# Performance work log

Hardware: AMD Instinct MI355X
Metric: run time of the kernel (lower is better)

## Reference

```python
import jax, jax.numpy as jnp
import numpy as np

WS = 7          # window_size
NH = 12         # num_heads
EPS = 1e-5      # LayerNorm eps


def setup_inputs() -> dict:
    key = jax.random.key(0)
    ks = jax.random.split(key, 8)
    B, H, W, C = 32, 56, 56, 384
    x = jax.random.normal(ks[0], (B, H * W, C), dtype=jnp.float32)
    s = 1.0 / np.sqrt(C)
    return {
        "x": x,
        "ln_gamma": jnp.ones((C,), jnp.float32),
        "ln_beta": jnp.zeros((C,), jnp.float32),
        "w_in": jax.random.normal(ks[1], (3 * C, C), jnp.float32) * s,   # torch in_proj_weight
        "b_in": jnp.zeros((3 * C,), jnp.float32),
        "w_out": jax.random.normal(ks[2], (C, C), jnp.float32) * s,      # torch out_proj.weight
        "b_out": jnp.zeros((C,), jnp.float32),
        "H": H,
        "W": W,
    }


def reference(x, ln_gamma, ln_beta, w_in, b_in, w_out, b_out, H, W):
    B, N, C = x.shape
    assert N == H * W
    hd = C // NH
    shortcut = x

    # LayerNorm
    mu = jnp.mean(x, axis=-1, keepdims=True)
    var = jnp.mean((x - mu) ** 2, axis=-1, keepdims=True)
    y = (x - mu) * jax.lax.rsqrt(var + EPS) * ln_gamma + ln_beta

    # window partition (pads are static Python ints)
    y = y.reshape(B, H, W, C)
    pad_h = (WS - H % WS) % WS
    pad_w = (WS - W % WS) % WS
    y = jnp.pad(y, ((0, 0), (0, pad_h), (0, pad_w), (0, 0)))
    Hp, Wp = H + pad_h, W + pad_w
    nh, nw = Hp // WS, Wp // WS
    y = y.reshape(B, nh, WS, nw, WS, C).transpose(0, 1, 3, 2, 4, 5)
    y = y.reshape(B * nh * nw, WS * WS, C)   # [NWIN, L, C]

    # MHA (torch nn.MultiheadAttention, batch_first)
    qkv = y @ w_in.T + b_in                   # [NWIN, L, 3C]
    q, k, v = jnp.split(qkv, 3, axis=-1)
    NWIN, L, _ = y.shape
    q = q.reshape(NWIN, L, NH, hd).transpose(0, 2, 1, 3)
    k = k.reshape(NWIN, L, NH, hd).transpose(0, 2, 1, 3)
    v = v.reshape(NWIN, L, NH, hd).transpose(0, 2, 1, 3)
    scores = jnp.einsum("whqd,whkd->whqk", q, k) / jnp.sqrt(jnp.float32(hd))
    attn = jax.nn.softmax(scores, axis=-1)
    o = jnp.einsum("whqk,whkd->whqd", attn, v)
    o = o.transpose(0, 2, 1, 3).reshape(NWIN, L, C)
    o = o @ w_out.T + b_out

    # window reverse + unpad + residual
    o = o.reshape(B, nh, nw, WS, WS, C).transpose(0, 1, 3, 2, 4, 5)
    o = o.reshape(B, Hp, Wp, C)[:, :H, :W, :].reshape(B, N, C)
    return shortcut + o
```

## Files before the change

### kernel.cpp

```cpp
#include <hip/hip_runtime.h>

typedef __bf16 bf16x8 __attribute__((ext_vector_type(8)));
typedef float f32x4 __attribute__((ext_vector_type(4)));
typedef unsigned short ushort8 __attribute__((ext_vector_type(8)));

#define LDS_AS(p) ((__attribute__((address_space(3))) void*)(p))
#define GLB_AS(p) ((const __attribute__((address_space(1))) void*)(p))

__device__ __forceinline__ unsigned short f2bf(float f) {
    union { float f; unsigned u; } v; v.f = f;
    unsigned r = v.u + 0x7fffu + ((v.u >> 16) & 1u);
    return (unsigned short)(r >> 16);
}

__global__ __launch_bounds__(256) void convw_kernel(
    const float* __restrict__ wi, const float* __restrict__ wo,
    unsigned short* __restrict__ qw, unsigned short* __restrict__ ow)
{
    const int i = blockIdx.x * 256 + threadIdx.x;
    if (i < 1152 * 384) qw[i] = f2bf(wi[i]);
    if (i < 384 * 384)  ow[i] = f2bf(wo[i]);
}

__global__ __launch_bounds__(256) void ln_kernel(
    const float* __restrict__ x, const float* __restrict__ gam,
    const float* __restrict__ bet, unsigned short* __restrict__ y)
{
    const int lane = threadIdx.x & 63;
    const int wv   = threadIdx.x >> 6;
    const int m    = blockIdx.x * 4 + wv;
    const int win  = m / 49, l = m - win * 49;
    const int b = win >> 6, wh = (win >> 3) & 7, ww = win & 7;
    const int i = l / 7, j = l - i * 7;
    const float2* xr = (const float2*)(x + ((size_t)b * 3136 + (wh * 7 + i) * 56 + (ww * 7 + j)) * 384);

    float2 v[3];
    float s = 0.f, ss = 0.f;
#pragma unroll
    for (int t = 0; t < 3; ++t) {
        v[t] = xr[t * 64 + lane];
        s  += v[t].x + v[t].y;
        ss += v[t].x * v[t].x + v[t].y * v[t].y;
    }
#pragma unroll
    for (int d = 1; d < 64; d <<= 1) {
        s  += __shfl_xor(s, d, 64);
        ss += __shfl_xor(ss, d, 64);
    }
    const float mu  = s * (1.f / 384.f);
    const float var = ss * (1.f / 384.f) - mu * mu;
    const float rs  = rsqrtf(var + 1e-5f);

    unsigned* yr = (unsigned*)(y + (size_t)m * 384);
#pragma unroll
    for (int t = 0; t < 3; ++t) {
        const int c = (t * 64 + lane) * 2;
        float a0 = (v[t].x - mu) * rs * gam[c]     + bet[c];
        float a1 = (v[t].y - mu) * rs * gam[c + 1] + bet[c + 1];
        yr[t * 64 + lane] = (unsigned)f2bf(a0) | ((unsigned)f2bf(a1) << 16);
    }
}

template <int N_, int EPI>
__global__ __launch_bounds__(256) void gemm_kernel(
    const unsigned short* __restrict__ A,
    const unsigned short* __restrict__ Bw,
    const float* __restrict__ bias,
    unsigned short* __restrict__ obf,
    const float* __restrict__ xres,
    float* __restrict__ oflt)
{
    __shared__ unsigned short As[128 * 32];
    __shared__ unsigned short Bs[128 * 32];
    const int lane = threadIdx.x & 63;
    const int wv   = threadIdx.x >> 6;
    const int m0 = blockIdx.y * 128;
    const int n0 = blockIdx.x * 128;
    const int wm = (wv & 1) * 64;
    const int wn = (wv >> 1) * 64;
    const int cl = lane & 15;
    const int qd = lane >> 4;
    const int srow = wv * 16 + (lane >> 2);
    const int scol = (lane & 3) * 8;

    f32x4 acc[4][4] = {};

    for (int kb = 0; kb < 12; ++kb) {
        const int k0 = kb * 32;
        __syncthreads();
#pragma unroll
        for (int t = 0; t < 2; ++t) {
            const unsigned short* ga = A  + (size_t)(m0 + t * 64 + srow) * 384 + k0 + scol;
            __builtin_amdgcn_global_load_lds(GLB_AS(ga), LDS_AS(As + (t * 64 + wv * 16) * 32), 16, 0, 0);
            const unsigned short* gb = Bw + (size_t)(n0 + t * 64 + srow) * 384 + k0 + scol;
            __builtin_amdgcn_global_load_lds(GLB_AS(gb), LDS_AS(Bs + (t * 64 + wv * 16) * 32), 16, 0, 0);
        }
        __syncthreads();

        bf16x8 af[4], bfr[4];
#pragma unroll
        for (int mt = 0; mt < 4; ++mt)
            af[mt] = *(const bf16x8*)(As + (wm + mt * 16 + cl) * 32 + qd * 8);
#pragma unroll
        for (int nt = 0; nt < 4; ++nt)
            bfr[nt] = *(const bf16x8*)(Bs + (wn + nt * 16 + cl) * 32 + qd * 8);
#pragma unroll
        for (int mt = 0; mt < 4; ++mt)
#pragma unroll
            for (int nt = 0; nt < 4; ++nt)
                acc[mt][nt] = __builtin_amdgcn_mfma_f32_16x16x32_bf16(af[mt], bfr[nt], acc[mt][nt], 0, 0, 0);
    }

#pragma unroll
    for (int mt = 0; mt < 4; ++mt) {
#pragma unroll
        for (int nt = 0; nt < 4; ++nt) {
            const int col = n0 + wn + nt * 16 + cl;
            const float bv = bias[col];
#pragma unroll
            for (int r = 0; r < 4; ++r) {
                const int m = m0 + wm + mt * 16 + qd * 4 + r;
                const float val = acc[mt][nt][r] + bv;
                if (EPI == 0) {
                    obf[(size_t)m * N_ + col] = f2bf(val);
                } else {
                    const int win = m / 49, l = m - win * 49;
                    const int b = win >> 6, wh = (win >> 3) & 7, ww = win & 7;
                    const int i = l / 7, j = l - i * 7;
                    const size_t sr = ((size_t)b * 3136 + (wh * 7 + i) * 56 + (ww * 7 + j)) * 384 + col;
                    oflt[sr] = xres[sr] + val;
                }
            }
        }
    }
}

__global__ __launch_bounds__(256) void attn_kernel(
    const unsigned short* __restrict__ qkv, unsigned short* __restrict__ o)
{
    __shared__ unsigned short P[4][64 * 72];
    const int lane = threadIdx.x & 63;
    const int wv   = threadIdx.x >> 6;
    const int cl = lane & 15;
    const int qd = lane >> 4;
    const int g   = blockIdx.x * 4 + wv;
    const int win = g / 12;
    const int h   = g - win * 12;
    const unsigned short* base = qkv + (size_t)win * (49 * 1152);

    bf16x8 aq[4], bk[4];
#pragma unroll
    for (int mt = 0; mt < 4; ++mt) {
        const int l = mt * 16 + cl;
        bf16x8 z = {};
        if (l < 49) z = *(const bf16x8*)(base + (size_t)l * 1152 + h * 32 + qd * 8);
        aq[mt] = z;
    }
#pragma unroll
    for (int nt = 0; nt < 4; ++nt) {
        const int lk = nt * 16 + cl;
        bf16x8 z = {};
        if (lk < 49) z = *(const bf16x8*)(base + (size_t)lk * 1152 + 384 + h * 32 + qd * 8);
        bk[nt] = z;
    }
    f32x4 s[4][4] = {};
#pragma unroll
    for (int mt = 0; mt < 4; ++mt)
#pragma unroll
        for (int nt = 0; nt < 4; ++nt)
            s[mt][nt] = __builtin_amdgcn_mfma_f32_16x16x32_bf16(aq[mt], bk[nt], s[mt][nt], 0, 0, 0);

    const float scale = 0.17677669529663687f;
#pragma unroll
    for (int mt = 0; mt < 4; ++mt)
#pragma unroll
        for (int nt = 0; nt < 4; ++nt)
#pragma unroll
            for (int r = 0; r < 4; ++r) {
                float t = s[mt][nt][r] * scale;
                if (nt * 16 + cl >= 49) t = -1e30f;
                s[mt][nt][r] = t;
            }

#pragma unroll
    for (int mt = 0; mt < 4; ++mt)
#pragma unroll
        for (int r = 0; r < 4; ++r) {
            float mx = fmaxf(fmaxf(s[mt][0][r], s[mt][1][r]), fmaxf(s[mt][2][r], s[mt][3][r]));
            mx = fmaxf(mx, __shfl_xor(mx, 1, 64));
            mx = fmaxf(mx, __shfl_xor(mx, 2, 64));
            mx = fmaxf(mx, __shfl_xor(mx, 4, 64));
            mx = fmaxf(mx, __shfl_xor(mx, 8, 64));
            float sm = 0.f;
#pragma unroll
            for (int nt = 0; nt < 4; ++nt) {
                const float p = __expf(s[mt][nt][r] - mx);
                s[mt][nt][r] = p;
                sm += p;
            }
            sm += __shfl_xor(sm, 1, 64);
            sm += __shfl_xor(sm, 2, 64);
            sm += __shfl_xor(sm, 4, 64);
            sm += __shfl_xor(sm, 8, 64);
            const float inv = 1.f / sm;
#pragma unroll
            for (int nt = 0; nt < 4; ++nt)
                s[mt][nt][r] *= inv;
        }

    unsigned short* Pw = &P[wv][0];
#pragma unroll
    for (int mt = 0; mt < 4; ++mt)
#pragma unroll
        for (int nt = 0; nt < 4; ++nt)
#pragma unroll
            for (int r = 0; r < 4; ++r)
                Pw[(mt * 16 + qd * 4 + r) * 72 + nt * 16 + cl] = f2bf(s[mt][nt][r]);

    f32x4 oa[4][2] = {};
    const unsigned short* vbase = base + 768 + h * 32;
#pragma unroll
    for (int kk = 0; kk < 2; ++kk) {
        bf16x8 ap[4];
#pragma unroll
        for (int mt = 0; mt < 4; ++mt)
            ap[mt] = *(const bf16x8*)(Pw + (mt * 16 + cl) * 72 + kk * 32 + qd * 8);
#pragma unroll
        for (int nt = 0; nt < 2; ++nt) {
            ushort8 tv;
#pragma unroll
            for (int jj = 0; jj < 8; ++jj) {
                const int lk = kk * 32 + qd * 8 + jj;
                tv[jj] = (lk < 49) ? vbase[(size_t)lk * 1152 + nt * 16 + cl] : (unsigned short)0;
            }
            const bf16x8 bv = __builtin_bit_cast(bf16x8, tv);
#pragma unroll
            for (int mt = 0; mt < 4; ++mt)
                oa[mt][nt] = __builtin_amdgcn_mfma_f32_16x16x32_bf16(ap[mt], bv, oa[mt][nt], 0, 0, 0);
        }
    }

    unsigned short* ob = o + (size_t)win * 49 * 384 + h * 32;
#pragma unroll
    for (int mt = 0; mt < 4; ++mt)
#pragma unroll
        for (int r = 0; r < 4; ++r) {
            const int l = mt * 16 + qd * 4 + r;
            if (l < 49) {
#pragma unroll
                for (int nt = 0; nt < 2; ++nt)
                    ob[(size_t)l * 384 + nt * 16 + cl] = f2bf(oa[mt][nt][r]);
            }
        }
}

extern "C" void kernel_launch(void* const* d_in, const int* in_sizes, int n_in,
                              void* d_out, int out_size, void* d_ws, size_t ws_size,
                              hipStream_t stream)
{
    const float* x   = (const float*)d_in[0];
    const float* gam = (const float*)d_in[1];
    const float* bet = (const float*)d_in[2];
    const float* wi  = (const float*)d_in[3];
    const float* bi  = (const float*)d_in[4];
    const float* wo  = (const float*)d_in[5];
    const float* bo  = (const float*)d_in[6];
    float* out = (float*)d_out;

    const int Bb   = in_sizes[0] / (3136 * 384);
    const int M    = Bb * 3136;
    const int NWIN = Bb * 64;

    char* ws = (char*)d_ws;
    unsigned short* qw   = (unsigned short*)(ws);
    unsigned short* ow   = (unsigned short*)(ws + 884736);
    unsigned short* y    = (unsigned short*)(ws + 1179648);
    unsigned short* qkv  = (unsigned short*)(ws + 1179648 + (size_t)M * 768);
    unsigned short* owin = (unsigned short*)(ws + 1179648 + (size_t)M * 768 + (size_t)M * 2304);

    convw_kernel<<<1728, 256, 0, stream>>>(wi, wo, qw, ow);
    ln_kernel<<<M / 4, 256, 0, stream>>>(x, gam, bet, y);
    gemm_kernel<1152, 0><<<dim3(9, M / 128), 256, 0, stream>>>(y, qw, bi, qkv, nullptr, nullptr);
    attn_kernel<<<NWIN * 12 / 4, 256, 0, stream>>>(qkv, owin);
    gemm_kernel<384, 1><<<dim3(3, M / 128), 256, 0, stream>>>(owin, ow, bo, nullptr, x, out);
}
```

Before: 625.5 us.

## Store V transposed per head from QKV GEMM, swizzle P in LDS, remap grid by XCD

The QKV GEMM epilogue now writes Q/K into a 768-wide buffer and V into a per-(window, head) transposed layout padded to 56 keys. The attention kernel can then load V fragments as contiguous 16-byte vectors instead of eight strided scalar loads. The P tile in LDS drops its padding and uses an XOR swizzle to avoid bank conflicts. Both GEMMs use a 1-D grid remapped so each XCD handles contiguous row blocks for L2 locality, and the attention output reuses the LN buffer. The scattered transposed V writes in the epilogue are uncoalesced, and padded V entries (l 49..55) are never written, so they depend on whatever is already in the workspace.

```diff
diff --git a/kernel.cpp b/kernel.cpp
--- a/kernel.cpp
+++ b/kernel.cpp
@@ -2,7 +2,6 @@
 
 typedef __bf16 bf16x8 __attribute__((ext_vector_type(8)));
 typedef float f32x4 __attribute__((ext_vector_type(4)));
-typedef unsigned short ushort8 __attribute__((ext_vector_type(8)));
 
 #define LDS_AS(p) ((__attribute__((address_space(3))) void*)(p))
 #define GLB_AS(p) ((const __attribute__((address_space(1))) void*)(p))
@@ -61,12 +60,13 @@
     }
 }
 
-template <int N_, int EPI>
+template <int NBX, int EPI>
 __global__ __launch_bounds__(256) void gemm_kernel(
     const unsigned short* __restrict__ A,
     const unsigned short* __restrict__ Bw,
     const float* __restrict__ bias,
     unsigned short* __restrict__ obf,
+    unsigned short* __restrict__ vt,
     const float* __restrict__ xres,
     float* __restrict__ oflt)
 {
@@ -74,8 +74,16 @@
     __shared__ unsigned short Bs[128 * 32];
     const int lane = threadIdx.x & 63;
     const int wv   = threadIdx.x >> 6;
-    const int m0 = blockIdx.y * 128;
-    const int n0 = blockIdx.x * 128;
+
+    const int id   = blockIdx.x;
+    const int xcd  = id & 7;
+    const int sl   = id >> 3;
+    const int gper = (gridDim.x >> 3) / NBX;
+    const int by   = xcd * gper + sl / NBX;
+    const int bx   = sl - (sl / NBX) * NBX;
+    const int m0 = by * 128;
+    const int n0 = bx * 128;
+
     const int wm = (wv & 1) * 64;
     const int wn = (wv >> 1) * 64;
     const int cl = lane & 15;
@@ -111,19 +119,17 @@
                 acc[mt][nt] = __builtin_amdgcn_mfma_f32_16x16x32_bf16(af[mt], bfr[nt], acc[mt][nt], 0, 0, 0);
     }
 
-#pragma unroll
-    for (int mt = 0; mt < 4; ++mt) {
-#pragma unroll
-        for (int nt = 0; nt < 4; ++nt) {
-            const int col = n0 + wn + nt * 16 + cl;
-            const float bv = bias[col];
-#pragma unroll
-            for (int r = 0; r < 4; ++r) {
-                const int m = m0 + wm + mt * 16 + qd * 4 + r;
-                const float val = acc[mt][nt][r] + bv;
-                if (EPI == 0) {
-                    obf[(size_t)m * N_ + col] = f2bf(val);
-                } else {
+    if (EPI == 1) {
+#pragma unroll
+        for (int mt = 0; mt < 4; ++mt)
+#pragma unroll
+            for (int nt = 0; nt < 4; ++nt) {
+                const int col = n0 + wn + nt * 16 + cl;
+                const float bv = bias[col];
+#pragma unroll
+                for (int r = 0; r < 4; ++r) {
+                    const int m = m0 + wm + mt * 16 + qd * 4 + r;
+                    const float val = acc[mt][nt][r] + bv;
                     const int win = m / 49, l = m - win * 49;
                     const int b = win >> 6, wh = (win >> 3) & 7, ww = win & 7;
                     const int i = l / 7, j = l - i * 7;
@@ -131,14 +137,44 @@
                     oflt[sr] = xres[sr] + val;
                 }
             }
-        }
+    } else if (n0 < 768) {
+#pragma unroll
+        for (int mt = 0; mt < 4; ++mt)
+#pragma unroll
+            for (int nt = 0; nt < 4; ++nt) {
+                const int col = n0 + wn + nt * 16 + cl;
+                const float bv = bias[col];
+#pragma unroll
+                for (int r = 0; r < 4; ++r) {
+                    const int m = m0 + wm + mt * 16 + qd * 4 + r;
+                    obf[(size_t)m * 768 + col] = f2bf(acc[mt][nt][r] + bv);
+                }
+            }
+    } else {
+#pragma unroll
+        for (int mt = 0; mt < 4; ++mt)
+#pragma unroll
+            for (int nt = 0; nt < 4; ++nt) {
+                const int col = n0 + wn + nt * 16 + cl;
+                const float bv = bias[col];
+                const int hcol = col - 768;
+                const int h = hcol >> 5, d = hcol & 31;
+#pragma unroll
+                for (int r = 0; r < 4; ++r) {
+                    const int m = m0 + wm + mt * 16 + qd * 4 + r;
+                    const int win = m / 49, l = m - win * 49;
+                    vt[((size_t)(win * 12 + h) * 32 + d) * 56 + l] = f2bf(acc[mt][nt][r] + bv);
+                }
+            }
     }
 }
 
 __global__ __launch_bounds__(256) void attn_kernel(
-    const unsigned short* __restrict__ qkv, unsigned short* __restrict__ o)
-{
-    __shared__ unsigned short P[4][64 * 72];
+    const unsigned short* __restrict__ qkv,
+    const unsigned short* __restrict__ vt,
+    unsigned short* __restrict__ o)
+{
+    __shared__ unsigned short P[4][64 * 64];
     const int lane = threadIdx.x & 63;
     const int wv   = threadIdx.x >> 6;
     const int cl = lane & 15;
@@ -146,21 +182,21 @@
     const int g   = blockIdx.x * 4 + wv;
     const int win = g / 12;
     const int h   = g - win * 12;
-    const unsigned short* base = qkv + (size_t)win * (49 * 1152);
+    const unsigned short* base = qkv + (size_t)win * (49 * 768);
 
     bf16x8 aq[4], bk[4];
 #pragma unroll
     for (int mt = 0; mt < 4; ++mt) {
         const int l = mt * 16 + cl;
         bf16x8 z = {};
-        if (l < 49) z = *(const bf16x8*)(base + (size_t)l * 1152 + h * 32 + qd * 8);
+        if (l < 49) z = *(const bf16x8*)(base + (size_t)l * 768 + h * 32 + qd * 8);
         aq[mt] = z;
     }
 #pragma unroll
     for (int nt = 0; nt < 4; ++nt) {
         const int lk = nt * 16 + cl;
         bf16x8 z = {};
-        if (lk < 49) z = *(const bf16x8*)(base + (size_t)lk * 1152 + 384 + h * 32 + qd * 8);
+        if (lk < 49) z = *(const bf16x8*)(base + (size_t)lk * 768 + 384 + h * 32 + qd * 8);
         bk[nt] = z;
     }
     f32x4 s[4][4] = {};
@@ -214,26 +250,27 @@
 #pragma unroll
         for (int nt = 0; nt < 4; ++nt)
 #pragma unroll
-            for (int r = 0; r < 4; ++r)
-                Pw[(mt * 16 + qd * 4 + r) * 72 + nt * 16 + cl] = f2bf(s[mt][nt][r]);
+            for (int r = 0; r < 4; ++r) {
+                const int row = mt * 16 + qd * 4 + r;
+                const int col = nt * 16 + cl;
+                const int cc  = (col >> 3) ^ (qd << 1);
+                Pw[row * 64 + cc * 8 + (col & 7)] = f2bf(s[mt][nt][r]);
+            }
 
     f32x4 oa[4][2] = {};
-    const unsigned short* vbase = base + 768 + h * 32;
+    const unsigned short* vb = vt + (size_t)(win * 12 + h) * (32 * 56);
+    const int key = (cl >> 2) & 3;
 #pragma unroll
     for (int kk = 0; kk < 2; ++kk) {
         bf16x8 ap[4];
 #pragma unroll
-        for (int mt = 0; mt < 4; ++mt)
-            ap[mt] = *(const bf16x8*)(Pw + (mt * 16 + cl) * 72 + kk * 32 + qd * 8);
+        for (int mt = 0; mt < 4; ++mt) {
+            const int cc = (kk * 4 + qd) ^ (key << 1);
+            ap[mt] = *(const bf16x8*)(Pw + (mt * 16 + cl) * 64 + cc * 8);
+        }
 #pragma unroll
         for (int nt = 0; nt < 2; ++nt) {
-            ushort8 tv;
-#pragma unroll
-            for (int jj = 0; jj < 8; ++jj) {
-                const int lk = kk * 32 + qd * 8 + jj;
-                tv[jj] = (lk < 49) ? vbase[(size_t)lk * 1152 + nt * 16 + cl] : (unsigned short)0;
-            }
-            const bf16x8 bv = __builtin_bit_cast(bf16x8, tv);
+            const bf16x8 bv = *(const bf16x8*)(vb + (nt * 16 + cl) * 56 + kk * 32 + qd * 8);
 #pragma unroll
             for (int mt = 0; mt < 4; ++mt)
                 oa[mt][nt] = __builtin_amdgcn_mfma_f32_16x16x32_bf16(ap[mt], bv, oa[mt][nt], 0, 0, 0);
@@ -276,11 +313,12 @@
     unsigned short* ow   = (unsigned short*)(ws + 884736);
     unsigned short* y    = (unsigned short*)(ws + 1179648);
     unsigned short* qkv  = (unsigned short*)(ws + 1179648 + (size_t)M * 768);
-    unsigned short* owin = (unsigned short*)(ws + 1179648 + (size_t)M * 768 + (size_t)M * 2304);
+    unsigned short* vt   = (unsigned short*)(ws + 1179648 + (size_t)M * 768 + (size_t)M * 1536);
+    unsigned short* owin = y;
 
     convw_kernel<<<1728, 256, 0, stream>>>(wi, wo, qw, ow);
     ln_kernel<<<M / 4, 256, 0, stream>>>(x, gam, bet, y);
-    gemm_kernel<1152, 0><<<dim3(9, M / 128), 256, 0, stream>>>(y, qw, bi, qkv, nullptr, nullptr);
-    attn_kernel<<<NWIN * 12 / 4, 256, 0, stream>>>(qkv, owin);
-    gemm_kernel<384, 1><<<dim3(3, M / 128), 256, 0, stream>>>(owin, ow, bo, nullptr, x, out);
-}
+    gemm_kernel<9, 0><<<(M / 128) * 9, 256, 0, stream>>>(y, qw, bi, qkv, vt, nullptr, nullptr);
+    attn_kernel<<<NWIN * 12 / 4, 256, 0, stream>>>(qkv, vt, owin);
+    gemm_kernel<3, 1><<<(M / 128) * 3, 256, 0, stream>>>(owin, ow, bo, nullptr, nullptr, x, out);
+}
```

New measurement: 654.3 us. +4.6%, slower.
